# Performance work log

Measured on AMD Instinct MI355X. Metric: run time of the kernel, lower is better.

## Reference

```python
import jax, jax.numpy as jnp
import numpy as np

K, D = 8, 32          # num_heads, node_out_dim
KD = K * D            # 256
NEG = 0.2             # LeakyReLU negative slope
N, E = 100000, 300000
DIN, DREL = 128, 64


def setup_inputs() -> dict:
    key = jax.random.key(0)
    ks = iter(jax.random.split(key, 64))
    def nrm(shape, scale):
        return jax.random.normal(next(ks), shape, jnp.float32) * scale
    inp = {}
    # per-relation target-node features feats[(s,e,d)] : (N_d, d_in)
    for nm in ["feat_ui", "feat_iu", "feat_ii", "feat_ii_rev"]:
        inp[nm] = nrm((N, DIN), 1.0)
    # relation input features (d_rel,)
    for nm in ["r_ui", "r_iu", "r_ii", "r_ii_rev"]:
        inp[nm] = nrm((DREL,), 1.0)
    # fc_node per ntype (no bias), shared for src/dst roles
    inp["W_user"] = nrm((DIN, KD), 0.05)
    inp["W_item"] = nrm((DIN, KD), 0.05)
    # fc_rel per etype (no bias): d_rel -> 2*K*d
    for nm in ["Wrel_ui", "Wrel_iu", "Wrel_ii", "Wrel_ii_rev"]:
        inp[nm] = nrm((DREL, 2 * KD), 0.05)
    # cross-relation attention vectors (K, d)
    for nm in ["attn_ui", "attn_iu", "attn_ii", "attn_ii_rev"]:
        inp[nm] = nrm((K, D), 0.1)
    # residual fc per ntype (with bias) and residual gate scalar
    inp["Wres_user"] = nrm((DIN, KD), 0.05); inp["bres_user"] = nrm((KD,), 0.02)
    inp["Wres_item"] = nrm((DIN, KD), 0.05); inp["bres_item"] = nrm((KD,), 0.02)
    inp["a_user"] = jax.random.uniform(next(ks), (1,), jnp.float32)
    inp["a_item"] = jax.random.uniform(next(ks), (1,), jnp.float32)
    # fc_upd per etype (with bias): d_rel -> K*rel_out
    for nm in ["ui", "iu", "ii", "ii_rev"]:
        inp["Wupd_" + nm] = nrm((DREL, KD), 0.05)
        inp["bupd_" + nm] = nrm((KD,), 0.02)
    # edge lists per relation
    for nm in ["ui", "iu", "ii", "ii_rev"]:
        inp["src_" + nm] = jax.random.randint(next(ks), (E,), 0, N, jnp.int32)
        inp["dst_" + nm] = jax.random.randint(next(ks), (E,), 0, N, jnp.int32)
    return inp


def _conv(fsrc_in, fdst_in, Ws, Wd, Wrel, rfeat, src, dst):
    """RelationGraphConv: GAT-style attention over one bipartite relation."""
    n_dst = fdst_in.shape[0]
    fs = (fsrc_in @ Ws).reshape(-1, K, D)          # (Ns, K, D)
    fd = (fdst_in @ Wd).reshape(-1, K, D)          # (Nd, K, D)
    attn = (rfeat @ Wrel).reshape(K, 2 * D)        # (K, 2D)
    el = (fs * attn[:, :D]).sum(-1)                # (Ns, K)
    er = (fd * attn[:, D:]).sum(-1)                # (Nd, K)
    e = jax.nn.leaky_relu(el[src] + er[dst], NEG)  # (E, K)
    # edge softmax per destination node
    m = jax.ops.segment_max(e, dst, num_segments=n_dst)
    ex = jnp.exp(e - m[dst])
    s = jax.ops.segment_sum(ex, dst, num_segments=n_dst)
    a = ex / s[dst]                                # (E, K)
    msg = fs[src] * a[:, :, None]                  # (E, K, D)
    out = jax.ops.segment_sum(msg, dst, num_segments=n_dst)
    return jax.nn.relu(out.reshape(n_dst, KD))     # activation = relu


def _crossing(stacked, rel_attn):
    """RelationCrossing over stacked per-relation dst reps (R, N, K*D)."""
    R, Nn = stacked.shape[0], stacked.shape[1]
    f = stacked.reshape(R, Nn, K, D)
    sc = (rel_attn * f).sum(-1, keepdims=True)             # (R, N, K, 1)
    sc = jax.nn.softmax(jax.nn.leaky_relu(sc, NEG), axis=0)
    return (sc * f).sum(0).reshape(Nn, KD)


def reference(feat_ui, feat_iu, feat_ii, feat_ii_rev,
              r_ui, r_iu, r_ii, r_ii_rev,
              W_user, W_item,
              Wrel_ui, Wrel_iu, Wrel_ii, Wrel_ii_rev,
              attn_ui, attn_iu, attn_ii, attn_ii_rev,
              Wres_user, bres_user, Wres_item, bres_item,
              a_user, a_item,
              Wupd_ui, bupd_ui, Wupd_iu, bupd_iu,
              Wupd_ii, bupd_ii, Wupd_ii_rev, bupd_ii_rev,
              src_ui, dst_ui, src_iu, dst_iu,
              src_ii, dst_ii, src_ii_rev, dst_ii_rev):
    # relation convs; src feats come from the reverse relation's dict entry
    h_ui = _conv(feat_iu, feat_ui, W_user, W_item, Wrel_ui, r_ui, src_ui, dst_ui)
    h_iu = _conv(feat_ui, feat_iu, W_item, W_user, Wrel_iu, r_iu, src_iu, dst_iu)
    h_ii = _conv(feat_ii_rev, feat_ii, W_item, W_item, Wrel_ii, r_ii, src_ii, dst_ii)
    h_iir = _conv(feat_ii, feat_ii_rev, W_item, W_item, Wrel_ii_rev, r_ii_rev, src_ii_rev, dst_ii_rev)

    # gated residual per dtype
    def resid(h, fdst, Wres, bres, a):
        al = jax.nn.sigmoid(a)
        return al * h + (1.0 - al) * (fdst @ Wres + bres)

    h_ui = resid(h_ui, feat_ui, Wres_item, bres_item, a_item)
    h_iu = resid(h_iu, feat_iu, Wres_user, bres_user, a_user)
    h_ii = resid(h_ii, feat_ii, Wres_item, bres_item, a_item)
    h_iir = resid(h_iir, feat_ii_rev, Wres_item, bres_item, a_item)

    # cross-relation fusion: dtype item has relations [ui, ii, ii_rev]; user has [iu]
    item_stack = jnp.stack([h_ui, h_ii, h_iir], axis=0)
    out_ui = _crossing(item_stack, attn_ui)
    out_iu = h_iu  # num_rel == 1 -> identity
    out_ii = _crossing(item_stack, attn_ii)
    out_iir = _crossing(item_stack, attn_ii_rev)

    # relation feature update
    ro_ui = r_ui @ Wupd_ui + bupd_ui
    ro_iu = r_iu @ Wupd_iu + bupd_iu
    ro_ii = r_ii @ Wupd_ii + bupd_ii
    ro_iir = r_ii_rev @ Wupd_ii_rev + bupd_ii_rev
    return (out_ui, out_iu, out_ii, out_iir, ro_ui, ro_iu, ro_ii, ro_iir)
```

## Files before the change

### kernel.cpp

```cpp
#include <hip/hip_runtime.h>
#include <hip/hip_bf16.h>
#include <math.h>

#define NEG_SLOPE 0.2f
#define LOG2E 1.4426950408889634f

using bf16x8 = __attribute__((ext_vector_type(8))) short;
using f32x4  = __attribute__((ext_vector_type(4))) float;
using u16x8  = __attribute__((ext_vector_type(8))) unsigned short;
using u16x4  = __attribute__((ext_vector_type(4))) unsigned short;

__device__ __forceinline__ float lrelu(float x) { return x > 0.f ? x : NEG_SLOPE * x; }
__device__ __forceinline__ float dot4(float4 a, float4 b) {
    return a.x * b.x + a.y * b.y + a.z * b.z + a.w * b.w;
}
__device__ __forceinline__ unsigned short f2b(float x) {
    union { float f; unsigned u; } v; v.f = x;
    unsigned r = v.u + 0x7fff + ((v.u >> 16) & 1);
    return (unsigned short)(r >> 16);
}
__device__ __forceinline__ float b2f(unsigned short b) {
    union { unsigned u; float f; } v; v.u = ((unsigned)b) << 16;
    return v.f;
}
__device__ __forceinline__ float4 load4b(const unsigned short* p) {
    u16x4 u = *reinterpret_cast<const u16x4*>(p);
    return make_float4(b2f(u[0]), b2f(u[1]), b2f(u[2]), b2f(u[3]));
}
__device__ __forceinline__ bf16x8 cvt8(float4 a0, float4 a1) {
    union { u16x8 u; bf16x8 b; } c;
    c.u[0] = f2b(a0.x); c.u[1] = f2b(a0.y); c.u[2] = f2b(a0.z); c.u[3] = f2b(a0.w);
    c.u[4] = f2b(a1.x); c.u[5] = f2b(a1.y); c.u[6] = f2b(a1.z); c.u[7] = f2b(a1.w);
    return c.b;
}

struct PackArgs {
    const float* W1[4];
    const float* W2[4];
    const float* wvA[4];
    const float* wvB[4];
    unsigned short* Bp[4];
};

__global__ __launch_bounds__(256)
void pack_b_k(PackArgs pa)
{
    const int r = blockIdx.y;
    const int nb = blockIdx.x;
    const int ks = threadIdx.x >> 6;
    const int lane = threadIdx.x & 63;
    const int n = nb * 16 + (lane & 15);
    const int k0 = ks * 32 + (lane >> 4) * 8;
    u16x8 u;
    if (n < 512) {
        const float* Wsrc = (n < 256) ? (pa.W1[r] + n) : (pa.W2[r] + (n - 256));
        #pragma unroll
        for (int e = 0; e < 8; ++e) u[e] = f2b(Wsrc[(size_t)(k0 + e) * 256]);
    } else {
        const int h = (n - 512) & 7;
        const bool isEr = (n >= 520);
        const float* wv = isEr ? (pa.wvB[r] + h * 64 + 32) : (pa.wvA[r] + h * 64);
        const float* Wc = pa.W1[r] + h * 32;
        #pragma unroll
        for (int e = 0; e < 8; ++e) {
            const size_t k = (size_t)(k0 + e);
            float s = 0.f;
            #pragma unroll 8
            for (int d = 0; d < 32; ++d) s = fmaf(Wc[k * 256 + d], wv[d], s);
            u[e] = f2b(s);
        }
    }
    const size_t gid = (size_t)((nb * 4 + ks) * 64 + lane);
    *reinterpret_cast<u16x8*>(pa.Bp[r] + gid * 8) = u;
}

struct GemmArgs {
    const float* A[4];
    const unsigned short* Bp[4];
    const float* bres[4];
    unsigned short* pool[4];
    unsigned short* resid[4];
    float* elOut[4];
    float* erOut[4];
};

__global__ __launch_bounds__(256)
void mfma_gemm_k(GemmArgs ga, int Nrows)
{
    __shared__ __align__(16) char smem[32768];
    const int rsel = blockIdx.y;
    const int t = threadIdx.x;
    const int wv = t >> 6, lane = t & 63;
    const int l15 = lane & 15, lg = lane >> 4;
    const int nloc = wv * 16 + l15;
    const int m0 = blockIdx.x * 64;
    const int node = m0 + nloc;
    const bool valid = node < Nrows;
    const int nc = valid ? node : (Nrows - 1);

    const float* __restrict__ A = ga.A[rsel];
    const unsigned short* __restrict__ Bp = ga.Bp[rsel];
    const float* __restrict__ bres = ga.bres[rsel];

    bf16x8 bfr[4];
    #pragma unroll
    for (int ks = 0; ks < 4; ++ks) {
        const float* p = A + (size_t)nc * 128 + ks * 32 + lg * 8;
        float4 a0 = *reinterpret_cast<const float4*>(p);
        float4 a1 = *reinterpret_cast<const float4*>(p + 4);
        bfr[ks] = cvt8(a0, a1);
    }

    const int swz = (nloc & 7) << 4;

    #pragma unroll
    for (int ni = 0; ni < 16; ++ni) {
        f32x4 acc = (f32x4){0.f, 0.f, 0.f, 0.f};
        #pragma unroll
        for (int ks = 0; ks < 4; ++ks) {
            bf16x8 wf = *reinterpret_cast<const bf16x8*>(
                Bp + ((size_t)((ni * 4 + ks) * 64 + lane)) * 8);
            acc = __builtin_amdgcn_mfma_f32_16x16x32_bf16(wf, bfr[ks], acc, 0, 0, 0);
        }
        u16x4 o;
        o[0] = f2b(acc[0]); o[1] = f2b(acc[1]); o[2] = f2b(acc[2]); o[3] = f2b(acc[3]);
        const int byte = nloc * 512 + ((ni * 32 + lg * 8) ^ swz);
        *reinterpret_cast<u16x4*>(smem + byte) = o;
    }
    __syncthreads();
    {
        unsigned short* __restrict__ dst = ga.pool[rsel];
        #pragma unroll
        for (int i = 0; i < 8; ++i) {
            const int chunk = i * 256 + t;
            const int row = chunk >> 5;
            const int c16 = chunk & 31;
            const int byte = row * 512 + ((c16 * 16) ^ ((row & 7) << 4));
            u16x8 v = *reinterpret_cast<const u16x8*>(smem + byte);
            if (m0 + row < Nrows)
                *reinterpret_cast<u16x8*>(dst + (size_t)(m0 + row) * 256 + c16 * 8) = v;
        }
    }
    __syncthreads();

    #pragma unroll
    for (int ni = 16; ni < 32; ++ni) {
        f32x4 acc = (f32x4){0.f, 0.f, 0.f, 0.f};
        #pragma unroll
        for (int ks = 0; ks < 4; ++ks) {
            bf16x8 wf = *reinterpret_cast<const bf16x8*>(
                Bp + ((size_t)((ni * 4 + ks) * 64 + lane)) * 8);
            acc = __builtin_amdgcn_mfma_f32_16x16x32_bf16(wf, bfr[ks], acc, 0, 0, 0);
        }
        const int cb = (ni - 16) * 16 + lg * 4;
        float4 bv = *reinterpret_cast<const float4*>(bres + cb);
        u16x4 o;
        o[0] = f2b(acc[0] + bv.x); o[1] = f2b(acc[1] + bv.y);
        o[2] = f2b(acc[2] + bv.z); o[3] = f2b(acc[3] + bv.w);
        const int byte = nloc * 512 + (((ni - 16) * 32 + lg * 8) ^ swz);
        *reinterpret_cast<u16x4*>(smem + byte) = o;
    }
    __syncthreads();
    {
        unsigned short* __restrict__ dst = ga.resid[rsel];
        #pragma unroll
        for (int i = 0; i < 8; ++i) {
            const int chunk = i * 256 + t;
            const int row = chunk >> 5;
            const int c16 = chunk & 31;
            const int byte = row * 512 + ((c16 * 16) ^ ((row & 7) << 4));
            u16x8 v = *reinterpret_cast<const u16x8*>(smem + byte);
            if (m0 + row < Nrows)
                *reinterpret_cast<u16x8*>(dst + (size_t)(m0 + row) * 256 + c16 * 8) = v;
        }
    }

    {
        f32x4 acc = (f32x4){0.f, 0.f, 0.f, 0.f};
        #pragma unroll
        for (int ks = 0; ks < 4; ++ks) {
            bf16x8 wf = *reinterpret_cast<const bf16x8*>(
                Bp + ((size_t)((32 * 4 + ks) * 64 + lane)) * 8);
            acc = __builtin_amdgcn_mfma_f32_16x16x32_bf16(wf, bfr[ks], acc, 0, 0, 0);
        }
        if (valid) {
            float4 v = make_float4(acc[0], acc[1], acc[2], acc[3]);
            if (lg < 2)
                *reinterpret_cast<float4*>(ga.elOut[rsel] + (size_t)node * 8 + lg * 4) = v;
            else
                *reinterpret_cast<float4*>(ga.erOut[rsel] + (size_t)node * 8 + (lg - 2) * 4) = v;
        }
    }
}

struct EdgePtrs {
    const int* src[4];
    const int* dst[4];
    int E[4];
    int csrOff[4];
};

__global__ __launch_bounds__(256)
void hist_k(EdgePtrs ep, int* __restrict__ counts4, int N)
{
    const int r = blockIdx.y;
    const int e = blockIdx.x * 256 + threadIdx.x;
    if (e < ep.E[r]) atomicAdd(counts4 + (size_t)r * N + ep.dst[r][e], 1);
}

__global__ __launch_bounds__(256)
void blksum_k(const int* __restrict__ counts4, int* __restrict__ blksum4, int N)
{
    const int r = blockIdx.y;
    const int* c = counts4 + (size_t)r * N;
    const int base = blockIdx.x * 1024 + threadIdx.x;
    int s = 0;
    #pragma unroll
    for (int i = 0; i < 4; ++i) { int idx = base + i * 256; if (idx < N) s += c[idx]; }
    __shared__ int sd[256];
    sd[threadIdx.x] = s; __syncthreads();
    for (int off = 128; off > 0; off >>= 1) {
        if (threadIdx.x < off) sd[threadIdx.x] += sd[threadIdx.x + off];
        __syncthreads();
    }
    if (threadIdx.x == 0) blksum4[r * 1024 + blockIdx.x] = sd[0];
}

__global__ __launch_bounds__(1024)
void scanblk_k(int* __restrict__ blksum4, int nbx)
{
    const int r = blockIdx.x;
    const int t = threadIdx.x;
    __shared__ int sd[1024];
    int v = (t < nbx) ? blksum4[r * 1024 + t] : 0;
    sd[t] = v; __syncthreads();
    for (int off = 1; off < 1024; off <<= 1) {
        int u = (t >= off) ? sd[t - off] : 0;
        __syncthreads();
        sd[t] += u;
        __syncthreads();
    }
    if (t < nbx) blksum4[r * 1024 + t] = sd[t] - v;
}

__global__ __launch_bounds__(256)
void cursor_k(const int* __restrict__ counts4, const int* __restrict__ blkoff4,
              int* __restrict__ cursor4, int N)
{
    const int r = blockIdx.y;
    const int* c = counts4 + (size_t)r * N;
    int* cur = cursor4 + (size_t)r * N;
    const int t = threadIdx.x;
    const int base = blockIdx.x * 1024 + t * 4;
    const int c0 = (base + 0 < N) ? c[base + 0] : 0;
    const int c1 = (base + 1 < N) ? c[base + 1] : 0;
    const int c2 = (base + 2 < N) ? c[base + 2] : 0;
    const int c3 = (base + 3 < N) ? c[base + 3] : 0;
    const int tsum = c0 + c1 + c2 + c3;
    __shared__ int sd[256];
    sd[t] = tsum; __syncthreads();
    for (int off = 1; off < 256; off <<= 1) {
        int u = (t >= off) ? sd[t - off] : 0;
        __syncthreads();
        sd[t] += u;
        __syncthreads();
    }
    int excl = sd[t] - tsum + blkoff4[r * 1024 + blockIdx.x];
    if (base + 0 < N) cur[base + 0] = excl;
    if (base + 1 < N) cur[base + 1] = excl + c0;
    if (base + 2 < N) cur[base + 2] = excl + c0 + c1;
    if (base + 3 < N) cur[base + 3] = excl + c0 + c1 + c2;
}

__global__ __launch_bounds__(256)
void scatter_k(EdgePtrs ep, int* __restrict__ cursor4, int* __restrict__ csr_src, int N)
{
    const int r = blockIdx.y;
    const int e = blockIdx.x * 256 + threadIdx.x;
    if (e < ep.E[r]) {
        const int d = ep.dst[r][e];
        const int pos = atomicAdd(cursor4 + (size_t)r * N + d, 1);
        csr_src[ep.csrOff[r] + pos] = ep.src[r][e];
    }
}

struct NodeArgs {
    const int* csr[4];
    const int* cursor[4];
    const int* counts[4];
    const float* el[4];
    const float* er[4];
    const unsigned short* pool[4];
    const unsigned short* resid[4];
};

__global__ __launch_bounds__(256)
void node_k(NodeArgs na,
            const float* __restrict__ attn_ui, const float* __restrict__ attn_ii,
            const float* __restrict__ attn_iir,
            const float* __restrict__ a_user, const float* __restrict__ a_item,
            float* __restrict__ out, int Nrows)
{
    const int lane = threadIdx.x & 63;
    const int n = blockIdx.x * 4 + (threadIdx.x >> 6);
    if (n >= Nrows) return;
    const int k = lane >> 3;

    int deg[4], endv[4];
    float erk[4];
    #pragma unroll
    for (int r = 0; r < 4; ++r) {
        deg[r]  = na.counts[r][n];
        endv[r] = na.cursor[r][n];
        erk[r]  = na.er[r][(size_t)n * 8 + k];
    }

    const float si = 1.f / (1.f + __expf(-a_item[0])), osi = 1.f - si;
    const float su = 1.f / (1.f + __expf(-a_user[0])), osu = 1.f - su;

    float4 fr[4];
    #pragma unroll
    for (int r = 0; r < 4; ++r) {
        const int d = deg[r];
        const int start = endv[r] - d;
        const int* __restrict__ csr = na.csr[r];
        const float* __restrict__ elr = na.el[r];
        const unsigned short* __restrict__ fs = na.pool[r];
        const float er_k = erk[r];
        float s = 0.f;
        float4 acc = make_float4(0.f, 0.f, 0.f, 0.f);
        for (int base = 0; base < d; base += 4) {
            const int m = d - base;
            int sidx[4];
            #pragma unroll
            for (int u = 0; u < 4; ++u)
                sidx[u] = csr[start + base + ((u < m) ? u : 0)];
            float ex[4];
            #pragma unroll
            for (int u = 0; u < 4; ++u) {
                const float x = elr[(size_t)sidx[u] * 8 + k] + er_k;
                const float e = __builtin_amdgcn_exp2f(fmaxf(x, NEG_SLOPE * x));
                ex[u] = (u < m) ? e : 0.f;
            }
            float4 pv[4];
            #pragma unroll
            for (int u = 0; u < 4; ++u)
                pv[u] = load4b(fs + (size_t)sidx[u] * 256 + lane * 4);
            #pragma unroll
            for (int u = 0; u < 4; ++u) {
                s += ex[u];
                acc.x = fmaf(pv[u].x, ex[u], acc.x);
                acc.y = fmaf(pv[u].y, ex[u], acc.y);
                acc.z = fmaf(pv[u].z, ex[u], acc.z);
                acc.w = fmaf(pv[u].w, ex[u], acc.w);
            }
        }
        const float inv = (d > 0) ? 1.f / s : 0.f;
        float4 R = load4b(na.resid[r] + (size_t)n * 256 + lane * 4);
        const float sg = (r == 1) ? su : si;
        const float og = (r == 1) ? osu : osi;
        fr[r].x = sg * fmaxf(acc.x * inv, 0.f) + og * R.x;
        fr[r].y = sg * fmaxf(acc.y * inv, 0.f) + og * R.y;
        fr[r].z = sg * fmaxf(acc.z * inv, 0.f) + og * R.z;
        fr[r].w = sg * fmaxf(acc.w * inv, 0.f) + og * R.w;
    }

    const float4 f0 = fr[0], f1 = fr[2], f2 = fr[3], fiu = fr[1];
    float4 w0 = *reinterpret_cast<const float4*>(attn_ui  + lane * 4);
    float4 w1 = *reinterpret_cast<const float4*>(attn_ii  + lane * 4);
    float4 w2 = *reinterpret_cast<const float4*>(attn_iir + lane * 4);

    float p[3][3];
    p[0][0] = dot4(w0, f0); p[0][1] = dot4(w0, f1); p[0][2] = dot4(w0, f2);
    p[1][0] = dot4(w1, f0); p[1][1] = dot4(w1, f1); p[1][2] = dot4(w1, f2);
    p[2][0] = dot4(w2, f0); p[2][1] = dot4(w2, f1); p[2][2] = dot4(w2, f2);
    #pragma unroll
    for (int x = 0; x < 3; ++x)
        #pragma unroll
        for (int r = 0; r < 3; ++r)
            #pragma unroll
            for (int m = 1; m < 8; m <<= 1)
                p[x][r] += __shfl_xor(p[x][r], m, 64);

    const size_t NK = (size_t)Nrows * 256;
    const size_t o = (size_t)n * 256 + lane * 4;
    const size_t xoff[3] = {0, 2 * NK, 3 * NK};
    #pragma unroll
    for (int x = 0; x < 3; ++x) {
        float a0 = lrelu(p[x][0]), a1 = lrelu(p[x][1]), a2 = lrelu(p[x][2]);
        float mx = fmaxf(a0, fmaxf(a1, a2));
        float e0 = __expf(a0 - mx), e1 = __expf(a1 - mx), e2 = __expf(a2 - mx);
        float inv = 1.f / (e0 + e1 + e2);
        e0 *= inv; e1 *= inv; e2 *= inv;
        float4 rr;
        rr.x = e0 * f0.x + e1 * f1.x + e2 * f2.x;
        rr.y = e0 * f0.y + e1 * f1.y + e2 * f2.y;
        rr.z = e0 * f0.z + e1 * f1.z + e2 * f2.z;
        rr.w = e0 * f0.w + e1 * f1.w + e2 * f2.w;
        *reinterpret_cast<float4*>(out + xoff[x] + o) = rr;
    }
    *reinterpret_cast<float4*>(out + NK + o) = fiu;
}

struct RelPtrs {
    const float* rf[4];
    const float* Wrel[4];
    const float* Wupd[4];
    const float* bupd[4];
};

__global__ __launch_bounds__(512)
void rel_k(RelPtrs P, float* __restrict__ wvec, float* __restrict__ ro)
{
    const int r = blockIdx.x;
    const int t = threadIdx.x;
    __shared__ float rfs[64];
    if (t < 64) rfs[t] = P.rf[r][t];
    __syncthreads();
    {
        const float* Wc = P.Wrel[r];
        float acc = 0.f;
        #pragma unroll 8
        for (int i = 0; i < 64; ++i) acc = fmaf(rfs[i], Wc[(size_t)i * 512 + t], acc);
        wvec[(size_t)r * 512 + t] = acc * LOG2E;
    }
    if (t < 256) {
        const float* Wc = P.Wupd[r];
        float acc = P.bupd[r][t];
        #pragma unroll 8
        for (int i = 0; i < 64; ++i) acc = fmaf(rfs[i], Wc[(size_t)i * 256 + t], acc);
        ro[(size_t)r * 256 + t] = acc;
    }
}

extern "C" void kernel_launch(void* const* d_in, const int* in_sizes, int n_in,
                              void* d_out, int out_size, void* d_ws, size_t ws_size,
                              hipStream_t stream)
{
    (void)n_in; (void)out_size; (void)ws_size;
    const float* feat_ui  = (const float*)d_in[0];
    const float* feat_iu  = (const float*)d_in[1];
    const float* feat_ii  = (const float*)d_in[2];
    const float* feat_iir = (const float*)d_in[3];
    const float* W_user   = (const float*)d_in[8];
    const float* W_item   = (const float*)d_in[9];
    const float* Wres_user = (const float*)d_in[18];
    const float* bres_user = (const float*)d_in[19];
    const float* Wres_item = (const float*)d_in[20];
    const float* bres_item = (const float*)d_in[21];
    const float* a_user = (const float*)d_in[22];
    const float* a_item = (const float*)d_in[23];
    const int N = in_sizes[0] / 128;
    const int Es[4] = {in_sizes[32], in_sizes[34], in_sizes[36], in_sizes[38]};
    int maxE = 0;
    for (int r = 0; r < 4; ++r) maxE = Es[r] > maxE ? Es[r] : maxE;

    const size_t NP = (size_t)N * 256;
    const size_t N8 = (size_t)N * 8;
    const size_t BPSZ = 33 * 4 * 64 * 8;

    unsigned short* us = (unsigned short*)d_ws;
    unsigned short* pool[4];
    unsigned short* resid[4];
    for (int r = 0; r < 4; ++r) pool[r]  = us + (size_t)r * NP;
    for (int r = 0; r < 4; ++r) resid[r] = us + (size_t)(4 + r) * NP;
    unsigned short* BpArr[4];
    for (int r = 0; r < 4; ++r) BpArr[r] = us + 8 * NP + (size_t)r * BPSZ;
    float* fl = (float*)(us + 8 * NP + 4 * BPSZ);
    float *el[4], *er[4];
    for (int r = 0; r < 4; ++r) { el[r] = fl + (size_t)(2 * r) * N8; er[r] = fl + (size_t)(2 * r + 1) * N8; }
    float* wvec = fl + 8 * N8;
    int* counts4 = (int*)(wvec + 4 * 512);
    int* cursor4 = counts4 + 4 * (size_t)N;
    int* blksum4 = cursor4 + 4 * (size_t)N;
    int* csr_src = blksum4 + 4 * 1024;
    float* out = (float*)d_out;

    EdgePtrs ep;
    {
        int off = 0;
        const int si[4] = {32, 34, 36, 38};
        for (int r = 0; r < 4; ++r) {
            ep.src[r] = (const int*)d_in[si[r]];
            ep.dst[r] = (const int*)d_in[si[r] + 1];
            ep.E[r] = Es[r];
            ep.csrOff[r] = off;
            off += Es[r];
        }
    }

    (void)hipMemsetAsync(counts4, 0, 4 * (size_t)N * sizeof(int), stream);

    RelPtrs rp;
    rp.rf[0]   = (const float*)d_in[4];  rp.rf[1]   = (const float*)d_in[5];
    rp.rf[2]   = (const float*)d_in[6];  rp.rf[3]   = (const float*)d_in[7];
    rp.Wrel[0] = (const float*)d_in[10]; rp.Wrel[1] = (const float*)d_in[11];
    rp.Wrel[2] = (const float*)d_in[12]; rp.Wrel[3] = (const float*)d_in[13];
    rp.Wupd[0] = (const float*)d_in[24]; rp.Wupd[1] = (const float*)d_in[26];
    rp.Wupd[2] = (const float*)d_in[28]; rp.Wupd[3] = (const float*)d_in[30];
    rp.bupd[0] = (const float*)d_in[25]; rp.bupd[1] = (const float*)d_in[27];
    rp.bupd[2] = (const float*)d_in[29]; rp.bupd[3] = (const float*)d_in[31];
    rel_k<<<dim3(4), dim3(512), 0, stream>>>(rp, wvec, out + 4 * NP);

    const int pair[4] = {1, 0, 3, 2};
    PackArgs pa;
    pa.W1[0] = W_user; pa.W2[0] = Wres_user;
    pa.W1[1] = W_item; pa.W2[1] = Wres_item;
    pa.W1[2] = W_item; pa.W2[2] = Wres_item;
    pa.W1[3] = W_item; pa.W2[3] = Wres_item;
    for (int r = 0; r < 4; ++r) {
        pa.wvA[r] = wvec + (size_t)r * 512;
        pa.wvB[r] = wvec + (size_t)pair[r] * 512;
        pa.Bp[r]  = BpArr[r];
    }
    pack_b_k<<<dim3(33, 4), 256, 0, stream>>>(pa);

    const int geb = (maxE + 255) / 256;
    const int nbx = (N + 1023) / 1024;
    hist_k<<<dim3(geb, 4), 256, 0, stream>>>(ep, counts4, N);
    blksum_k<<<dim3(nbx, 4), 256, 0, stream>>>(counts4, blksum4, N);
    scanblk_k<<<dim3(4), 1024, 0, stream>>>(blksum4, nbx);
    cursor_k<<<dim3(nbx, 4), 256, 0, stream>>>(counts4, blksum4, cursor4, N);
    scatter_k<<<dim3(geb, 4), 256, 0, stream>>>(ep, cursor4, csr_src, N);

    GemmArgs ga;
    ga.A[0] = feat_iu;  ga.bres[0] = bres_user;
    ga.A[1] = feat_ui;  ga.bres[1] = bres_item;
    ga.A[2] = feat_iir; ga.bres[2] = bres_item;
    ga.A[3] = feat_ii;  ga.bres[3] = bres_item;
    for (int r = 0; r < 4; ++r) {
        ga.Bp[r]    = BpArr[r];
        ga.pool[r]  = pool[r];
        ga.resid[r] = resid[pair[r]];
        ga.elOut[r] = el[r];
        ga.erOut[r] = er[pair[r]];
    }
    const int gb = (N + 63) / 64;
    mfma_gemm_k<<<dim3(gb, 4), 256, 0, stream>>>(ga, N);

    NodeArgs na;
    for (int r = 0; r < 4; ++r) {
        na.csr[r]    = csr_src + ep.csrOff[r];
        na.cursor[r] = cursor4 + (size_t)r * N;
        na.counts[r] = counts4 + (size_t)r * N;
        na.el[r]     = el[r];
        na.er[r]     = er[r];
        na.pool[r]   = pool[r];
        na.resid[r]  = resid[r];
    }
    const int nb4 = (N + 3) / 4;
    node_k<<<nb4, 256, 0, stream>>>(na,
                                    (const float*)d_in[14], (const float*)d_in[16],
                                    (const float*)d_in[17],
                                    a_user, a_item, out, N);
}
```

Measured before the change: 665.5 us.

## Stage GEMM weight panels through LDS with register prefetch double-buffering

Weight fragments that each wave previously read directly from global memory are now loaded cooperatively in 32KB panels into an LDS slab. The next panel is prefetched into registers while MFMAs consume the current one. This cuts redundant per-wave global or L2 weight traffic across the four waves. In exchange, LDS doubles to 64KB per block, which may lower occupancy, and more barriers are added.

Result: faster. 571.6 us (-14.1%).

```diff
diff --git a/kernel.cpp b/kernel.cpp
--- a/kernel.cpp
+++ b/kernel.cpp
@@ -87,7 +87,9 @@
 __global__ __launch_bounds__(256)
 void mfma_gemm_k(GemmArgs ga, int Nrows)
 {
-    __shared__ __align__(16) char smem[32768];
+    __shared__ __align__(16) char smem[65536];
+    unsigned short* slab = (unsigned short*)smem;
+    char* bounce = smem + 32768;
     const int rsel = blockIdx.y;
     const int t = threadIdx.x;
     const int wv = t >> 6, lane = t & 63;
@@ -113,74 +115,87 @@
 
     const int swz = (nloc & 7) << 4;
 
-    #pragma unroll
-    for (int ni = 0; ni < 16; ++ni) {
-        f32x4 acc = (f32x4){0.f, 0.f, 0.f, 0.f};
-        #pragma unroll
-        for (int ks = 0; ks < 4; ++ks) {
-            bf16x8 wf = *reinterpret_cast<const bf16x8*>(
-                Bp + ((size_t)((ni * 4 + ks) * 64 + lane)) * 8);
-            acc = __builtin_amdgcn_mfma_f32_16x16x32_bf16(wf, bfr[ks], acc, 0, 0, 0);
-        }
-        u16x4 o;
-        o[0] = f2b(acc[0]); o[1] = f2b(acc[1]); o[2] = f2b(acc[2]); o[3] = f2b(acc[3]);
-        const int byte = nloc * 512 + ((ni * 32 + lg * 8) ^ swz);
-        *reinterpret_cast<u16x4*>(smem + byte) = o;
-    }
-    __syncthreads();
+    u16x8 sreg[8];
+    #pragma unroll
+    for (int j = 0; j < 8; ++j)
+        sreg[j] = *reinterpret_cast<const u16x8*>(Bp + (size_t)(j * 256 + t) * 8);
+
+    u16x8 snext;
+
+    #pragma unroll
+    for (int p = 0; p < 4; ++p) {
+        #pragma unroll
+        for (int j = 0; j < 8; ++j)
+            *reinterpret_cast<u16x8*>(slab + (size_t)(j * 256 + t) * 8) = sreg[j];
+        __syncthreads();
+        if (p < 3) {
+            const unsigned short* src = Bp + (size_t)(p + 1) * 16384;
+            #pragma unroll
+            for (int j = 0; j < 8; ++j)
+                sreg[j] = *reinterpret_cast<const u16x8*>(src + (size_t)(j * 256 + t) * 8);
+        } else {
+            snext = *reinterpret_cast<const u16x8*>(Bp + (size_t)65536 + (size_t)t * 8);
+        }
+        const bool isPool = (p < 2);
+        #pragma unroll
+        for (int i = 0; i < 8; ++i) {
+            const int ni = p * 8 + i;
+            f32x4 acc = (f32x4){0.f, 0.f, 0.f, 0.f};
+            #pragma unroll
+            for (int ks = 0; ks < 4; ++ks) {
+                bf16x8 wf = *reinterpret_cast<const bf16x8*>(
+                    slab + (size_t)((i * 4 + ks) * 64 + lane) * 8);
+                acc = __builtin_amdgcn_mfma_f32_16x16x32_bf16(wf, bfr[ks], acc, 0, 0, 0);
+            }
+            const int cni = isPool ? ni : (ni - 16);
+            u16x4 o;
+            if (isPool) {
+                o[0] = f2b(acc[0]); o[1] = f2b(acc[1]);
+                o[2] = f2b(acc[2]); o[3] = f2b(acc[3]);
+            } else {
+                float4 bv = *reinterpret_cast<const float4*>(bres + cni * 16 + lg * 4);
+                o[0] = f2b(acc[0] + bv.x); o[1] = f2b(acc[1] + bv.y);
+                o[2] = f2b(acc[2] + bv.z); o[3] = f2b(acc[3] + bv.w);
+            }
+            *reinterpret_cast<u16x4*>(bounce + nloc * 512 + ((cni * 32 + lg * 8) ^ swz)) = o;
+        }
+        __syncthreads();
+        if (p == 1) {
+            unsigned short* __restrict__ dst = ga.pool[rsel];
+            #pragma unroll
+            for (int i = 0; i < 8; ++i) {
+                const int chunk = i * 256 + t;
+                const int row = chunk >> 5;
+                const int c16 = chunk & 31;
+                const int byte = row * 512 + ((c16 * 16) ^ ((row & 7) << 4));
+                u16x8 v = *reinterpret_cast<const u16x8*>(bounce + byte);
+                if (m0 + row < Nrows)
+                    *reinterpret_cast<u16x8*>(dst + (size_t)(m0 + row) * 256 + c16 * 8) = v;
+            }
+            __syncthreads();
+        }
+    }
+    *reinterpret_cast<u16x8*>(slab + (size_t)t * 8) = snext;
     {
-        unsigned short* __restrict__ dst = ga.pool[rsel];
+        unsigned short* __restrict__ dst = ga.resid[rsel];
         #pragma unroll
         for (int i = 0; i < 8; ++i) {
             const int chunk = i * 256 + t;
             const int row = chunk >> 5;
             const int c16 = chunk & 31;
             const int byte = row * 512 + ((c16 * 16) ^ ((row & 7) << 4));
-            u16x8 v = *reinterpret_cast<const u16x8*>(smem + byte);
+            u16x8 v = *reinterpret_cast<const u16x8*>(bounce + byte);
             if (m0 + row < Nrows)
                 *reinterpret_cast<u16x8*>(dst + (size_t)(m0 + row) * 256 + c16 * 8) = v;
         }
     }
     __syncthreads();
-
-    #pragma unroll
-    for (int ni = 16; ni < 32; ++ni) {
+    {
         f32x4 acc = (f32x4){0.f, 0.f, 0.f, 0.f};
         #pragma unroll
         for (int ks = 0; ks < 4; ++ks) {
             bf16x8 wf = *reinterpret_cast<const bf16x8*>(
-                Bp + ((size_t)((ni * 4 + ks) * 64 + lane)) * 8);
-            acc = __builtin_amdgcn_mfma_f32_16x16x32_bf16(wf, bfr[ks], acc, 0, 0, 0);
-        }
-        const int cb = (ni - 16) * 16 + lg * 4;
-        float4 bv = *reinterpret_cast<const float4*>(bres + cb);
-        u16x4 o;
-        o[0] = f2b(acc[0] + bv.x); o[1] = f2b(acc[1] + bv.y);
-        o[2] = f2b(acc[2] + bv.z); o[3] = f2b(acc[3] + bv.w);
-        const int byte = nloc * 512 + (((ni - 16) * 32 + lg * 8) ^ swz);
-        *reinterpret_cast<u16x4*>(smem + byte) = o;
-    }
-    __syncthreads();
-    {
-        unsigned short* __restrict__ dst = ga.resid[rsel];
-        #pragma unroll
-        for (int i = 0; i < 8; ++i) {
-            const int chunk = i * 256 + t;
-            const int row = chunk >> 5;
-            const int c16 = chunk & 31;
-            const int byte = row * 512 + ((c16 * 16) ^ ((row & 7) << 4));
-            u16x8 v = *reinterpret_cast<const u16x8*>(smem + byte);
-            if (m0 + row < Nrows)
-                *reinterpret_cast<u16x8*>(dst + (size_t)(m0 + row) * 256 + c16 * 8) = v;
-        }
-    }
-
-    {
-        f32x4 acc = (f32x4){0.f, 0.f, 0.f, 0.f};
-        #pragma unroll
-        for (int ks = 0; ks < 4; ++ks) {
-            bf16x8 wf = *reinterpret_cast<const bf16x8*>(
-                Bp + ((size_t)((32 * 4 + ks) * 64 + lane)) * 8);
+                slab + (size_t)(ks * 64 + lane) * 8);
             acc = __builtin_amdgcn_mfma_f32_16x16x32_bf16(wf, bfr[ks], acc, 0, 0, 0);
         }
         if (valid) {
```
